# Kernel tuning notes

Measured on AMD Instinct MI355X. Metric: run time of the kernel, lower is better.

## Reference

```python
import jax, jax.numpy as jnp
import numpy as np

D = 128; T = 128; E = 100; H = 2
B = 2048; N0 = 3 * B; K0 = 5; N1 = N0 * K0; K1 = 10
NN = 200000; M = 4096; MSG = 2 * D + E + T  # 484


def t2v(t, w, b):
    # Time2Vec: cos(t * w + b), output [..., T]
    return jnp.cos(t[..., None] * w + b)


def gru_cell(x, h, Wih, bih, Whh, bhh):
    gi = x @ Wih.T + bih
    gh = h @ Whh.T + bhh
    ir, iz, inn = jnp.split(gi, 3, axis=-1)
    hr, hz, hn = jnp.split(gh, 3, axis=-1)
    r = jax.nn.sigmoid(ir + hr)
    u = jax.nn.sigmoid(iz + hz)
    n = jnp.tanh(inn + r * hn)
    return (1.0 - u) * n + u * h


def temporal_attn(node_feat, time_feat, edge_feat, nbr_feat, nbr_time_feat, mask,
                  Wq, bq, Wk, bk, Wv, bv, Wo, bo):
    N = node_feat.shape[0]
    q = (jnp.concatenate([node_feat, time_feat], -1) @ Wq + bq).reshape(N, H, D // H)
    kin = jnp.concatenate([nbr_feat, edge_feat, nbr_time_feat], -1)  # [N, K, D+E+T]
    k = (kin @ Wk + bk).reshape(N, -1, H, D // H)
    v = (kin @ Wv + bv).reshape(N, -1, H, D // H)
    s = jnp.einsum('nhd,nkhd->nhk', q, k) / jnp.sqrt(jnp.asarray(D // H, q.dtype))
    s = jnp.where(mask[:, None, :] > 0, s, jnp.asarray(-1e9, s.dtype))
    a = jax.nn.softmax(s, axis=-1)
    hout = jnp.einsum('nhk,nkhd->nhd', a, v).reshape(N, D)
    return jax.nn.relu(jnp.concatenate([hout, node_feat], -1) @ Wo + bo)


def setup_inputs() -> dict:
    key = jax.random.key(0)
    ks = jax.random.split(key, 60)
    it = iter(range(60))
    nx = lambda: ks[next(it)]
    p = lambda shape: jax.random.normal(nx(), shape, jnp.float32) * 0.05
    inp = dict(memory=p((NN, D)), time_w=p((T,)), time_b=p((T,)),
               gru_Wih=p((3 * D, MSG)), gru_bih=p((3 * D,)),
               gru_Whh=p((3 * D, D)), gru_bhh=p((3 * D,)))
    for l in (0, 1):
        inp['Wq%d' % l] = p((D + T, D)); inp['bq%d' % l] = p((D,))
        inp['Wk%d' % l] = p((D + E + T, D)); inp['bk%d' % l] = p((D,))
        inp['Wv%d' % l] = p((D + E + T, D)); inp['bv%d' % l] = p((D,))
        inp['Wo%d' % l] = p((2 * D, D)); inp['bo%d' % l] = p((D,))
    inp.update(lp_Ws=p((D, D)), lp_bs=p((D,)), lp_Wd=p((D, D)), lp_bd=p((D,)),
               lp_Wo=p((D, 1)), lp_bo=p((1,)))
    inp['msgs'] = jax.random.normal(nx(), (M, MSG), jnp.float32)
    inp['times0'] = jax.random.uniform(nx(), (N0,), jnp.float32) * 100.0 + 100.0
    inp['nbr_times0'] = inp['times0'][:, None] - jax.random.uniform(nx(), (N0, K0), jnp.float32) * 100.0
    inp['nbr_feats0'] = jax.random.normal(nx(), (N0, K0, E), jnp.float32)
    inp['times1'] = jax.random.uniform(nx(), (N1,), jnp.float32) * 100.0 + 100.0
    inp['nbr_times1'] = inp['times1'][:, None] - jax.random.uniform(nx(), (N1, K1), jnp.float32) * 100.0
    inp['nbr_feats1'] = jax.random.normal(nx(), (N1, K1, E), jnp.float32)
    inp['msg_nids'] = jax.random.permutation(nx(), NN)[:M].astype(jnp.int32)
    inp['seed0'] = jax.random.randint(nx(), (N0,), 0, NN, jnp.int32)
    inp['seed1'] = jax.random.randint(nx(), (N1,), 0, NN, jnp.int32)
    inp['nbr_local0'] = (N0 + jax.random.randint(nx(), (N0, K0), 0, N1)).astype(jnp.int32)
    inp['nbr_mask0'] = jax.random.randint(nx(), (N0, K0), 0, 2, jnp.int32).at[:, 0].set(1)
    inp['nbr_mask1'] = jax.random.randint(nx(), (N1, K1), 0, 2, jnp.int32).at[:, 0].set(1)
    inp['src_local'] = jax.random.randint(nx(), (B,), 0, N0, jnp.int32)
    inp['dst_local'] = jax.random.randint(nx(), (B,), 0, N0, jnp.int32)
    inp['neg_local'] = jax.random.randint(nx(), (B,), 0, N0, jnp.int32)
    return inp


def reference(memory, time_w, time_b, gru_Wih, gru_bih, gru_Whh, gru_bhh,
              Wq0, bq0, Wk0, bk0, Wv0, bv0, Wo0, bo0,
              Wq1, bq1, Wk1, bk1, Wv1, bv1, Wo1, bo1,
              lp_Ws, lp_bs, lp_Wd, lp_bd, lp_Wo, lp_bo,
              msgs, times0, nbr_times0, nbr_feats0, times1, nbr_times1, nbr_feats1,
              msg_nids, seed0, seed1, nbr_local0, nbr_mask0, nbr_mask1,
              src_local, dst_local, neg_local):
    # GRU memory update on aggregated messages (get_updated_memory)
    mem = memory.at[msg_nids].set(
        gru_cell(msgs, memory[msg_nids], gru_Wih, gru_bih, gru_Whh, gru_bhh))
    z = jnp.zeros((N0 + N1, D), jnp.float32)
    # hop 1 (outermost): neighbor node features are zeros
    tf1 = t2v(jnp.zeros((N1,), jnp.float32), time_w, time_b)
    ntf1 = t2v(times1[:, None] - nbr_times1, time_w, time_b)
    out1 = temporal_attn(mem[seed1], tf1, nbr_feats1,
                         jnp.zeros((N1, K1, D), jnp.float32), ntf1, nbr_mask1,
                         Wq1, bq1, Wk1, bk1, Wv1, bv1, Wo1, bo1)
    z = z.at[N0 + jnp.arange(N1)].set(out1)
    # hop 0: gather neighbor embeddings from hop-1 results
    tf0 = t2v(jnp.zeros((N0,), jnp.float32), time_w, time_b)
    ntf0 = t2v(times0[:, None] - nbr_times0, time_w, time_b)
    out0 = temporal_attn(mem[seed0], tf0, nbr_feats0, z[nbr_local0], ntf0, nbr_mask0,
                         Wq0, bq0, Wk0, bk0, Wv0, bv0, Wo0, bo0)
    z = z.at[jnp.arange(N0)].set(out0)
    z_src, z_dst, z_neg = z[src_local], z[dst_local], z[neg_local]

    def link_pred(a, c):
        hh = jax.nn.relu(a @ lp_Ws + lp_bs + c @ lp_Wd + lp_bd)
        return jax.nn.sigmoid(hh @ lp_Wo + lp_bo).ravel()

    return link_pred(z_src, z_dst), link_pred(z_src, z_neg)
```

## Files before the change

kernel.cpp:

```cpp
#include <hip/hip_runtime.h>
#include <math.h>

#define D    128
#define TT   128
#define E    100
#define NHD  2
#define BSZ  2048
#define N0C  6144
#define K0C  5
#define N1C  30720
#define K1C  10
#define NNC  200000
#define MC   4096
#define MSG  484
#define KIN  356
#define GK   612
#define GKP  616
#define GN   512

typedef __attribute__((ext_vector_type(8))) short short8v;
typedef __attribute__((ext_vector_type(4))) float f32x4;

__device__ __forceinline__ float sigmoidf_(float x){ return 1.f/(1.f+__expf(-x)); }
__device__ __forceinline__ unsigned short f2b(float f){
    unsigned int x = __float_as_uint(f);
    unsigned int r = (x + 0x7fffu + ((x>>16)&1u)) >> 16;
    return (unsigned short)r;
}
__device__ __forceinline__ float b2f(unsigned short u){
    return __uint_as_float(((unsigned int)u)<<16);
}
__device__ __forceinline__ void pin4(float4& v){
    float a=v.x, b=v.y, c=v.z, d=v.w;
    asm volatile("" : "+v"(a), "+v"(b), "+v"(c), "+v"(d));
    v.x=a; v.y=b; v.z=c; v.w=d;
}

__global__ void k_pre_small(const float* time_b,
                            const float* Wq0,const float* bq0,const float* Wq1,const float* bq1,
                            const float* bv0,const float* Wo0,const float* bo0,
                            const float* bv1,const float* Wo1,const float* bo1,
                            const float* bih,const float* bhh,float* gBias,
                            float* qc0, float* qc1, float* cb0, float* cb1){
    __shared__ float cosb[TT];
    int j = threadIdx.x;
    if(j < TT) cosb[j] = cosf(time_b[j]);
    __syncthreads();
    if(j < 128){
        float a0=bq0[j], a1=bq1[j];
        for(int t=0;t<TT;++t){ a0 += cosb[t]*Wq0[(D+t)*D + j]; a1 += cosb[t]*Wq1[(D+t)*D + j]; }
        qc0[j]=a0; qc1[j]=a1;
        float c0=bo0[j], c1=bo1[j];
        for(int jp=0;jp<D;++jp){ c0 += bv0[jp]*Wo0[jp*D + j]; c1 += bv1[jp]*Wo1[jp*D + j]; }
        cb0[j]=c0; cb1[j]=c1;
    }
    if(j < GN){
        float v;
        if(j < 256)      v = bih[j] + bhh[j];
        else if(j < 384) v = bih[j];
        else             v = bhh[j-128];
        gBias[j] = v;
    }
}

__global__ void k_wf(const float* Wq,const float* Wk,const float* bk,const float* qc,
                     unsigned short* WF, float* cF, int cmin){
    int span = 356 - cmin;
    int hstr = span + 4;
    int width = 2*hstr;
    int idx = blockIdx.x;
    int h = idx / hstr; int cl = idx % hstr;
    int k = threadIdx.x;
    if(cl > span){
        WF[(size_t)k*width + idx] = (unsigned short)0;
        if(k==0) cF[idx] = 0.f;
        return;
    }
    int c = cmin + cl;
    float a = 0.f;
    for(int d=0; d<64; ++d){
        float wkv = (c < KIN) ? Wk[c*D + h*64+d] : bk[h*64+d];
        a += Wq[k*D + h*64+d] * wkv;
    }
    WF[(size_t)k*width + idx] = f2b(a);
    if(k==0){
        float s=0.f;
        for(int d=0; d<64; ++d){
            float wkv = (c < KIN) ? Wk[c*D + h*64+d] : bk[h*64+d];
            s += qc[h*64+d]*wkv;
        }
        cF[idx] = s;
    }
}

__global__ void k_bcat(const float* Wv, const float* Wo, unsigned short* Bcat, int cmin){
    int span = KIN - cmin; int rows = 2*span;
    int r = blockIdx.x; int j = threadIdx.x;
    float a;
    if(r < rows){
        int h = r/span; int c = cmin + (r - h*span);
        a = 0.f;
        for(int d=0; d<64; ++d) a += Wv[c*D + h*64+d] * Wo[(h*64+d)*D + j];
    } else {
        a = Wo[(size_t)(D + (r - rows))*D + j];
    }
    Bcat[(size_t)r*D + j] = f2b(a);
}

__global__ __launch_bounds__(256) void k_gruB(const float* Wih, const float* Whh, unsigned short* B){
    __shared__ float tile[64][65];
    int rb = blockIdx.x*64;
    int jb = blockIdx.y*64;
    int t = threadIdx.x;
    int rr = t&63, jj0 = t>>6;
    #pragma unroll
    for(int i=0;i<16;++i){
        int jj = jj0 + i*4;
        int j = jb + jj; int r = rb + rr;
        float v = 0.f;
        if(r < GK){
            if(j < 256)      v = (r<MSG)? Wih[(size_t)j*MSG+r] : Whh[(size_t)j*D + (r-MSG)];
            else if(j < 384) v = (r<MSG)? Wih[(size_t)j*MSG+r] : 0.f;
            else             v = (r<MSG)? 0.f : Whh[(size_t)(j-128)*D + (r-MSG)];
        }
        tile[jj][rr] = v;
    }
    __syncthreads();
    int jw = t&63, rr0 = t>>6;
    #pragma unroll
    for(int i=0;i<16;++i){
        int rr2 = rr0 + i*4;
        int r = rb + rr2;
        if(r < GK) B[(size_t)r*GN + jb + jw] = f2b(tile[jw][rr2]);
    }
}
__global__ void k_acvt(const float* msgs, const float* memory, const int* msg_nids,
                       unsigned short* ab, float* hprevf, int* map){
    int i = blockIdx.x*256 + threadIdx.x;
    if(i >= MC*GKP) return;
    int row = i / GKP; int c = i - row*GKP;
    if(c == 0) map[msg_nids[row]] = row;
    float v;
    if(c < MSG) v = msgs[(size_t)row*MSG + c];
    else if(c < GK){ int d = c-MSG; v = memory[(size_t)msg_nids[row]*D + d]; hprevf[row*D+d] = v; }
    else v = 0.f;
    ab[i] = f2b(v);
}
__global__ void k_gates3(const float* part, const float* bias, const float* hprevf, float* upd){
    int i = blockIdx.x*256 + threadIdx.x;
    if(i >= MC*D) return;
    int row = i>>7, d = i&127;
    const float* p = part + (size_t)row*GN;
    const size_t S = (size_t)MC*GN;
    float gr = p[d]     + p[S+d]     + p[2*S+d]     + bias[d];
    float gu = p[128+d] + p[S+128+d] + p[2*S+128+d] + bias[128+d];
    float gi = p[256+d] + p[S+256+d] + p[2*S+256+d] + bias[256+d];
    float gh = p[384+d] + p[S+384+d] + p[2*S+384+d] + bias[384+d];
    float r = sigmoidf_(gr);
    float u = sigmoidf_(gu);
    float n = tanhf(gi + r*gh);
    upd[i] = (1.f-u)*n + u*hprevf[i];
}

__global__ void k_gatherf(const int* seed1,const int* seed0,const int* map,const int* msg_nids,
                          const float* memory,const float* upd,
                          unsigned short* hb1, unsigned short* acat1,
                          unsigned short* hb0, unsigned short* acat0){
    int i = blockIdx.x*256 + threadIdx.x;
    const int total1 = N1C*D;
    int li; const int* seed; unsigned short* hb; unsigned short* acat; int ldav, hoff;
    if(i < total1){ li=i; seed=seed1; hb=hb1; acat=acat1; ldav=584; hoff=456; }
    else { li = i - total1; if(li >= N0C*D) return; seed=seed0; hb=hb0; acat=acat0; ldav=840; hoff=712; }
    int row = li>>7, c = li&127;
    int sid = seed[row];
    int mi = map[sid];
    bool valid = ((unsigned)mi < (unsigned)MC) && (msg_nids[mi] == sid);
    float v = valid ? upd[(size_t)mi*D + c] : memory[(size_t)sid*D + c];
    unsigned short u = f2b(v);
    hb[li] = u;
    acat[(size_t)row*ldav + hoff + c] = u;
}

template<int BM, int SPLITK, bool RELU, bool OUTF32>
__global__ __launch_bounds__(256) void k_gmm(const unsigned short* A, int lda,
                                             const unsigned short* B, int ldb,
                                             const float* bias, void* Cp, int ldc,
                                             int K, int N, int M){
    constexpr int ASTR = 72;
    constexpr int BSTR = 72;
    constexpr int RPW = BM/4;
    constexpr int RT  = RPW/16;
    constexpr int AIT = BM/32;
    __shared__ unsigned short As[BM*ASTR];
    __shared__ unsigned short Bs[64*BSTR];
    int t = threadIdx.x;
    int wave = t>>6, lane = t&63;
    int l15 = lane&15, l4 = lane>>4;
    int m0 = blockIdx.y*BM, n0 = blockIdx.x*64;
    int ntiles = (K+63)>>6;
    int tbeg, tend;
    if(SPLITK==1){ tbeg=0; tend=ntiles; }
    else {
        int tper = (ntiles + SPLITK-1)/SPLITK;
        tbeg = blockIdx.z*tper;
        tend = min(ntiles, tbeg+tper);
    }
    f32x4 acc[RT][4];
    #pragma unroll
    for(int rt=0;rt<RT;++rt)
        #pragma unroll
        for(int ct=0;ct<4;++ct) acc[rt][ct] = (f32x4){0.f,0.f,0.f,0.f};

    uint4 apre[AIT]; unsigned short bpre[16];
    auto loadA = [&](int kt){
        int k0 = kt<<6;
        #pragma unroll
        for(int i=0;i<AIT;++i){
            int idx = t + i*256;
            int row = idx>>3; int kc = (idx&7)*8;
            uint4 v = {0u,0u,0u,0u};
            if(k0+kc < K) v = *(const uint4*)(A + (size_t)(m0+row)*lda + k0 + kc);
            apre[i] = v;
        }
    };
    auto loadB = [&](int kt){
        int k0 = kt<<6;
        int n = t&63; int kb = (t>>6)*16;
        int ng = n0+n;
        #pragma unroll
        for(int j=0;j<16;++j){
            int kg = k0 + kb + j;
            bpre[j] = (kg<K && ng<N) ? B[(size_t)kg*ldb + ng] : (unsigned short)0;
        }
    };
    auto stash = [&](){
        #pragma unroll
        for(int i=0;i<AIT;++i){
            int idx = t + i*256;
            int row = idx>>3; int kc = (idx&7)*8;
            *(uint4*)&As[row*ASTR + kc] = apre[i];
        }
        int n = t&63; int kb = (t>>6)*16;
        #pragma unroll
        for(int j=0;j<16;++j) Bs[n*BSTR + kb + j] = bpre[j];
    };

    loadA(tbeg); loadB(tbeg);
    for(int kt=tbeg; kt<tend; ++kt){
        stash();
        __syncthreads();
        if(kt+1 < tend){ loadA(kt+1); loadB(kt+1); }
        #pragma unroll
        for(int kk=0; kk<64; kk+=32){
            short8v bfr[4];
            #pragma unroll
            for(int ct=0;ct<4;++ct)
                bfr[ct] = *(const short8v*)&Bs[(ct*16+l15)*BSTR + kk + l4*8];
            #pragma unroll
            for(int rt=0;rt<RT;++rt){
                short8v afr = *(const short8v*)&As[(wave*RPW + rt*16 + l15)*ASTR + kk + l4*8];
                #pragma unroll
                for(int ct=0;ct<4;++ct)
                    acc[rt][ct] = __builtin_amdgcn_mfma_f32_16x16x32_bf16(afr, bfr[ct], acc[rt][ct], 0,0,0);
            }
        }
        __syncthreads();
    }
    #pragma unroll
    for(int rt=0;rt<RT;++rt){
        #pragma unroll
        for(int ct=0;ct<4;++ct){
            int col = n0 + ct*16 + l15;
            if(col < N){
                #pragma unroll
                for(int r=0;r<4;++r){
                    int row = m0 + wave*RPW + rt*16 + l4*4 + r;
                    if(SPLITK==1){
                        float v = acc[rt][ct][r] + bias[col];
                        if(RELU) v = fmaxf(v, 0.f);
                        if(OUTF32) ((float*)Cp)[(size_t)row*ldc + col] = v;
                        else ((unsigned short*)Cp)[(size_t)row*ldc + col] = f2b(v);
                    } else {
                        ((float*)Cp)[((size_t)blockIdx.z*M + row)*ldc + col] = acc[rt][ct][r];
                    }
                }
            }
        }
    }
}

template<int SPL, bool RELU, bool OUTF32>
__global__ void k_kred(const float* part, int M, int N, const float* bias, void* out){
    int i = blockIdx.x*256 + threadIdx.x;
    if(i >= M*N) return;
    int col = i & (N-1);
    float v = bias[col];
    #pragma unroll
    for(int z=0;z<SPL;++z) v += part[(size_t)z*M*N + i];
    if(RELU) v = fmaxf(v, 0.f);
    if(OUTF32) ((float*)out)[i] = v;
    else ((unsigned short*)out)[i] = f2b(v);
}

template<int K, int CMIN, int S4, int NPW>
__global__ __launch_bounds__(256,4) void k_attn(const unsigned short* __restrict__ qwb,
    unsigned short* __restrict__ avout, int ldav,
    const float* __restrict__ times, const float* __restrict__ nbr_times,
    const float* __restrict__ nbr_feats,
    const int* __restrict__ nbr_mask, const int* __restrict__ nbr_local,
    const unsigned short* __restrict__ zbuf,
    const float* __restrict__ time_w, const float* __restrict__ time_b){
    constexpr int SPAN = KIN - CMIN;
    constexpr int QSTR = SPAN + 4;
    constexpr int QLD  = 2*QSTR;
    int wv = __builtin_amdgcn_readfirstlane(blockIdx.x*4 + (threadIdx.x>>6));
    int lane = threadIdx.x & 63;

    float4 tw4[S4], tb4[S4];
    #pragma unroll
    for(int s=0;s<S4;++s){
        int c = CMIN + s*256 + lane*4;
        if(c >= D+E && c < KIN){
            tw4[s] = *(const float4*)(time_w + (c-(D+E)));
            tb4[s] = *(const float4*)(time_b + (c-(D+E)));
        } else {
            tw4[s] = make_float4(0.f,0.f,0.f,0.f);
            tb4[s] = make_float4(0.f,0.f,0.f,0.f);
        }
    }

    #pragma unroll
    for(int i=0;i<NPW;++i){
        int n = wv*NPW + i;
        const unsigned short* qrow = qwb + (size_t)n*QLD;
        float tn = times[n];
        int   mk[K]; float tk[K]; int nl[K];
        #pragma unroll
        for(int k=0;k<K;++k){
            mk[k] = nbr_mask [(size_t)n*K + k];
            tk[k] = nbr_times[(size_t)n*K + k];
            nl[k] = (CMIN==0) ? nbr_local[(size_t)n*K + k] : 0;
        }

        float4 qw4[NHD][S4]; float qb[NHD];
        #pragma unroll
        for(int h=0;h<NHD;++h){
            qb[h] = b2f(qrow[h*QSTR + SPAN]);
            #pragma unroll
            for(int s=0;s<S4;++s){
                int cl = s*256 + lane*4;
                float4 v = make_float4(0.f,0.f,0.f,0.f);
                if(cl < SPAN){
                    uint2 wq = *(const uint2*)(qrow + h*QSTR + cl);
                    v.x = __uint_as_float(wq.x<<16);
                    v.y = __uint_as_float(wq.x & 0xffff0000u);
                    v.z = __uint_as_float(wq.y<<16);
                    v.w = __uint_as_float(wq.y & 0xffff0000u);
                }
                pin4(v);
                qw4[h][s] = v;
            }
        }

        float4 kin4[K][S4];
        #pragma unroll
        for(int k=0;k<K;++k){
            int gk = (mk[k] > 0) ? k : 0;
            float dt = tn - tk[gk];
            const float* ef = nbr_feats + (size_t)(n*K+gk)*E;
            const unsigned short* zf = (CMIN==0) ?
                (zbuf + (size_t)(nl[gk] - N0C)*D) : (const unsigned short*)0;
            #pragma unroll
            for(int s=0;s<S4;++s){
                int c = CMIN + s*256 + lane*4;
                float4 kv = make_float4(0.f,0.f,0.f,0.f);
                if(c < KIN){
                    if(CMIN==0 && c < D){
                        uint2 wz = *(const uint2*)(zf + c);
                        kv.x = __uint_as_float(wz.x<<16);
                        kv.y = __uint_as_float(wz.x & 0xffff0000u);
                        kv.z = __uint_as_float(wz.y<<16);
                        kv.w = __uint_as_float(wz.y & 0xffff0000u);
                    } else if(c < D+E){
                        kv = *(const float4*)(ef + (c-D));
                    } else {
                        kv.x = __cosf(dt*tw4[s].x + tb4[s].x);
                        kv.y = __cosf(dt*tw4[s].y + tb4[s].y);
                        kv.z = __cosf(dt*tw4[s].z + tb4[s].z);
                        kv.w = __cosf(dt*tw4[s].w + tb4[s].w);
                    }
                }
                pin4(kv);
                kin4[k][s] = kv;
            }
        }

        float p0[K], p1[K];
        #pragma unroll
        for(int k=0;k<K;++k){ p0[k]=0.f; p1[k]=0.f; }
        #pragma unroll
        for(int k=0;k<K;++k){
            if(mk[k] > 0){
                float a0 = 0.f, a1 = 0.f;
                #pragma unroll
                for(int s=0;s<S4;++s){
                    float4 kv = kin4[k][s];
                    a0 += kv.x*qw4[0][s].x + kv.y*qw4[0][s].y + kv.z*qw4[0][s].z + kv.w*qw4[0][s].w;
                    a1 += kv.x*qw4[1][s].x + kv.y*qw4[1][s].y + kv.z*qw4[1][s].z + kv.w*qw4[1][s].w;
                }
                p0[k] = a0; p1[k] = a1;
            }
        }

        #pragma unroll
        for(int off=32; off; off>>=1){
            #pragma unroll
            for(int k=0;k<K;++k){
                if(mk[k] > 0){
                    p0[k] += __shfl_xor(p0[k], off);
                    p1[k] += __shfl_xor(p1[k], off);
                }
            }
        }

        float sval[NHD][K];
        #pragma unroll
        for(int k=0;k<K;++k){
            bool act = mk[k] > 0;
            sval[0][k] = act ? (p0[k] + qb[0])*0.125f : -1e9f;
            sval[1][k] = act ? (p1[k] + qb[1])*0.125f : -1e9f;
        }
        #pragma unroll
        for(int h=0;h<NHD;++h){
            float mx = -1e30f;
            #pragma unroll
            for(int k=0;k<K;++k) mx = fmaxf(mx, sval[h][k]);
            float z=0.f;
            #pragma unroll
            for(int k=0;k<K;++k){ float e = __expf(sval[h][k]-mx); sval[h][k]=e; z+=e; }
            float inv = 1.f/z;
            #pragma unroll
            for(int k=0;k<K;++k) sval[h][k]*=inv;
        }

        #pragma unroll
        for(int s=0;s<S4;++s){
            int cl = s*256 + lane*4;
            if(cl < SPAN){
                float a00=0.f,a01=0.f,a02=0.f,a03=0.f;
                float a10=0.f,a11=0.f,a12=0.f,a13=0.f;
                #pragma unroll
                for(int k=0;k<K;++k){
                    if(mk[k] > 0){
                        float4 kv = kin4[k][s];
                        float w0 = sval[0][k], w1 = sval[1][k];
                        a00 += w0*kv.x; a01 += w0*kv.y; a02 += w0*kv.z; a03 += w0*kv.w;
                        a10 += w1*kv.x; a11 += w1*kv.y; a12 += w1*kv.z; a13 += w1*kv.w;
                    }
                }
                uint2 o0, o1;
                o0.x = (unsigned int)f2b(a00) | ((unsigned int)f2b(a01)<<16);
                o0.y = (unsigned int)f2b(a02) | ((unsigned int)f2b(a03)<<16);
                o1.x = (unsigned int)f2b(a10) | ((unsigned int)f2b(a11)<<16);
                o1.y = (unsigned int)f2b(a12) | ((unsigned int)f2b(a13)<<16);
                *(uint2*)(avout + (size_t)n*ldav + cl)        = o0;
                *(uint2*)(avout + (size_t)n*ldav + SPAN + cl) = o1;
            }
        }
    }
}

__global__ __launch_bounds__(128) void k_linkpred(const float* z0,
      const int* src,const int* dst,const int* neg,
      const float* Ws,const float* bs,const float* Wd,const float* bd,
      const float* Wo,const float* bo, float* out){
    __shared__ float zs[D], zd[D], zn[D];
    __shared__ float red[4];
    int b = blockIdx.x; int d = threadIdx.x;
    zs[d] = z0[(size_t)src[b]*D + d];
    zd[d] = z0[(size_t)dst[b]*D + d];
    zn[d] = z0[(size_t)neg[b]*D + d];
    __syncthreads();
    float ss=0.f, sdd=0.f, snn=0.f;
    for(int c=0;c<D;++c){
        float w1 = Ws[c*D + d], w2 = Wd[c*D + d];
        ss  += zs[c]*w1; sdd += zd[c]*w2; snn += zn[c]*w2;
    }
    float bb = bs[d] + bd[d];
    float h1 = fmaxf(ss + sdd + bb, 0.f);
    float h2 = fmaxf(ss + snn + bb, 0.f);
    float w = Wo[d];
    float v1 = h1*w, v2 = h2*w;
    #pragma unroll
    for(int off=32; off; off>>=1){ v1 += __shfl_xor(v1,off); v2 += __shfl_xor(v2,off); }
    int wid = d>>6;
    if((d&63)==0){ red[wid*2]=v1; red[wid*2+1]=v2; }
    __syncthreads();
    if(d==0){
        out[b]       = sigmoidf_(red[0]+red[2] + bo[0]);
        out[BSZ + b] = sigmoidf_(red[1]+red[3] + bo[0]);
    }
}

extern "C" void kernel_launch(void* const* d_in, const int* in_sizes, int n_in,
                              void* d_out, int out_size, void* d_ws, size_t ws_size,
                              hipStream_t stream) {
    const float* memory  = (const float*)d_in[0];
    const float* time_w  = (const float*)d_in[1];
    const float* time_b  = (const float*)d_in[2];
    const float* gWih    = (const float*)d_in[3];
    const float* gbih    = (const float*)d_in[4];
    const float* gWhh    = (const float*)d_in[5];
    const float* gbhh    = (const float*)d_in[6];
    const float* Wq0=(const float*)d_in[7],  *bq0=(const float*)d_in[8];
    const float* Wk0=(const float*)d_in[9],  *bk0=(const float*)d_in[10];
    const float* Wv0=(const float*)d_in[11], *bv0=(const float*)d_in[12];
    const float* Wo0=(const float*)d_in[13], *bo0=(const float*)d_in[14];
    const float* Wq1=(const float*)d_in[15], *bq1=(const float*)d_in[16];
    const float* Wk1=(const float*)d_in[17], *bk1=(const float*)d_in[18];
    const float* Wv1=(const float*)d_in[19], *bv1=(const float*)d_in[20];
    const float* Wo1=(const float*)d_in[21], *bo1=(const float*)d_in[22];
    const float* lpWs=(const float*)d_in[23], *lpbs=(const float*)d_in[24];
    const float* lpWd=(const float*)d_in[25], *lpbd=(const float*)d_in[26];
    const float* lpWo=(const float*)d_in[27], *lpbo=(const float*)d_in[28];
    const float* msgs    = (const float*)d_in[29];
    const float* times0  = (const float*)d_in[30];
    const float* ntimes0 = (const float*)d_in[31];
    const float* nfeats0 = (const float*)d_in[32];
    const float* times1  = (const float*)d_in[33];
    const float* ntimes1 = (const float*)d_in[34];
    const float* nfeats1 = (const float*)d_in[35];
    const int* msg_nids  = (const int*)d_in[36];
    const int* seed0     = (const int*)d_in[37];
    const int* seed1     = (const int*)d_in[38];
    const int* nbr_local0= (const int*)d_in[39];
    const int* nbr_mask0 = (const int*)d_in[40];
    const int* nbr_mask1 = (const int*)d_in[41];
    const int* src       = (const int*)d_in[42];
    const int* dst       = (const int*)d_in[43];
    const int* neg       = (const int*)d_in[44];

    char* ws = (char*)d_ws;
    size_t off = 0;
    auto alloc = [&](size_t bytes)->char*{
        char* p = ws + off;
        off += (bytes + 255) & ~(size_t)255;
        return p;
    };
    int*   map   = (int*)  alloc((size_t)NNC*4);
    float* upd   = (float*)alloc((size_t)MC*D*4);
    unsigned short* hb1   = (unsigned short*)alloc((size_t)N1C*D*2);
    unsigned short* qwb1  = (unsigned short*)alloc((size_t)N1C*464*2);
    unsigned short* acat1 = (unsigned short*)alloc((size_t)N1C*584*2);
    unsigned short* zb1   = (unsigned short*)alloc((size_t)N1C*D*2);
    unsigned short* hb0   = (unsigned short*)alloc((size_t)N0C*D*2);
    unsigned short* qwb0  = (unsigned short*)alloc((size_t)N0C*720*2);
    unsigned short* acat0 = (unsigned short*)alloc((size_t)N0C*840*2);
    float* z0    = (float*)alloc((size_t)N0C*D*4);
    float* qc0   = (float*)alloc(512);
    float* qc1   = (float*)alloc(512);
    float* cb0   = (float*)alloc(512);
    float* cb1   = (float*)alloc(512);
    unsigned short* WFb0 = (unsigned short*)alloc((size_t)D*720*2);
    unsigned short* WFb1 = (unsigned short*)alloc((size_t)D*464*2);
    float* cF0   = (float*)alloc((size_t)720*4);
    float* cF1   = (float*)alloc((size_t)464*4);
    unsigned short* Bcat1 = (unsigned short*)alloc((size_t)584*D*2);
    unsigned short* Bcat0 = (unsigned short*)alloc((size_t)840*D*2);
    unsigned short* gA    = (unsigned short*)alloc((size_t)MC*GKP*2);
    unsigned short* gB    = (unsigned short*)alloc((size_t)GK*GN*2);
    float* gBias = (float*)alloc((size_t)GN*4);
    float* hprevf= (float*)alloc((size_t)MC*D*4);
    float* part  = (float*)alloc((size_t)2*N1C*D*4);
    float* outp = (float*)d_out;

    k_pre_small<<<1,512,0,stream>>>(time_b, Wq0,bq0,Wq1,bq1, bv0,Wo0,bo0, bv1,Wo1,bo1,
                                    gbih, gbhh, gBias, qc0,qc1,cb0,cb1);
    k_wf<<<720,128,0,stream>>>(Wq0,Wk0,bk0,qc0, WFb0,cF0, 0);
    k_wf<<<464,128,0,stream>>>(Wq1,Wk1,bk1,qc1, WFb1,cF1, 128);
    k_bcat<<<584,128,0,stream>>>(Wv1, Wo1, Bcat1, 128);
    k_bcat<<<840,128,0,stream>>>(Wv0, Wo0, Bcat0, 0);
    k_gruB<<<dim3(10,8),256,0,stream>>>(gWih, gWhh, gB);

    k_acvt<<<(MC*GKP+255)/256,256,0,stream>>>(msgs, memory, msg_nids, gA, hprevf, map);
    k_gmm<128,3,false,true><<<dim3(GN/64, MC/128, 3),256,0,stream>>>(gA,GKP, gB,GN, gBias, part,GN, GK, GN, MC);
    k_gates3<<<(MC*D+255)/256,256,0,stream>>>(part, gBias, hprevf, upd);

    k_gatherf<<<((N1C+N0C)*D)/256,256,0,stream>>>(seed1, seed0, map, msg_nids, memory, upd,
                                                  hb1, acat1, hb0, acat0);

    k_gmm<128,1,false,false><<<dim3(8,  N1C/128),256,0,stream>>>(hb1,128, WFb1,464, cF1, qwb1,464, 128, 464, N1C);
    k_gmm<128,1,false,false><<<dim3(12, N0C/128),256,0,stream>>>(hb0,128, WFb0,720, cF0, qwb0,720, 128, 720, N0C);

    k_attn<K1C,128,1,1><<<N1C/4,256,0,stream>>>(qwb1, acat1, 584, times1, ntimes1, nfeats1,
                                                nbr_mask1, (const int*)0, (const unsigned short*)0,
                                                time_w, time_b);
    k_gmm<128,2,true,false><<<dim3(2, N1C/128, 2),256,0,stream>>>(acat1,584, Bcat1,D, cb1, part,D, 584, D, N1C);
    k_kred<2,true,false><<<(N1C*D+255)/256,256,0,stream>>>(part, N1C, D, cb1, zb1);

    k_attn<K0C,0,2,1><<<N0C/4,256,0,stream>>>(qwb0, acat0, 840, times0, ntimes0, nfeats0,
                                              nbr_mask0, nbr_local0, zb1,
                                              time_w, time_b);
    k_gmm<64,4,true,true><<<dim3(2, N0C/64, 4),256,0,stream>>>(acat0,840, Bcat0,D, cb0, part,D, 840, D, N0C);
    k_kred<4,true,true><<<(N0C*D+255)/256,256,0,stream>>>(part, N0C, D, cb0, z0);

    k_linkpred<<<BSZ,128,0,stream>>>(z0, src,dst,neg, lpWs,lpbs,lpWd,lpbd, lpWo,lpbo, outp);
}
```

Before: 583.4 us.

## Simplify attention kernel register use and drop split-K for hop-1 output GEMM

```diff
diff --git a/kernel.cpp b/kernel.cpp
--- a/kernel.cpp
+++ b/kernel.cpp
@@ -29,11 +29,6 @@
 }
 __device__ __forceinline__ float b2f(unsigned short u){
     return __uint_as_float(((unsigned int)u)<<16);
-}
-__device__ __forceinline__ void pin4(float4& v){
-    float a=v.x, b=v.y, c=v.z, d=v.w;
-    asm volatile("" : "+v"(a), "+v"(b), "+v"(c), "+v"(d));
-    v.x=a; v.y=b; v.z=c; v.w=d;
 }
 
 __global__ void k_pre_small(const float* time_b,
@@ -303,7 +298,7 @@
 }
 
 template<int K, int CMIN, int S4, int NPW>
-__global__ __launch_bounds__(256,4) void k_attn(const unsigned short* __restrict__ qwb,
+__global__ __launch_bounds__(256) void k_attn(const unsigned short* __restrict__ qwb,
     unsigned short* __restrict__ avout, int ldav,
     const float* __restrict__ times, const float* __restrict__ nbr_times,
     const float* __restrict__ nbr_feats,
@@ -357,7 +352,6 @@
                     v.z = __uint_as_float(wq.y<<16);
                     v.w = __uint_as_float(wq.y & 0xffff0000u);
                 }
-                pin4(v);
                 qw4[h][s] = v;
             }
         }
@@ -365,11 +359,10 @@
         float4 kin4[K][S4];
         #pragma unroll
         for(int k=0;k<K;++k){
-            int gk = (mk[k] > 0) ? k : 0;
-            float dt = tn - tk[gk];
-            const float* ef = nbr_feats + (size_t)(n*K+gk)*E;
+            float dt = tn - tk[k];
+            const float* ef = nbr_feats + (size_t)(n*K+k)*E;
             const unsigned short* zf = (CMIN==0) ?
-                (zbuf + (size_t)(nl[gk] - N0C)*D) : (const unsigned short*)0;
+                (zbuf + (size_t)(nl[k] - N0C)*D) : (const unsigned short*)0;
             #pragma unroll
             for(int s=0;s<S4;++s){
                 int c = CMIN + s*256 + lane*4;
@@ -390,36 +383,29 @@
                         kv.w = __cosf(dt*tw4[s].w + tb4[s].w);
                     }
                 }
-                pin4(kv);
                 kin4[k][s] = kv;
             }
         }
 
         float p0[K], p1[K];
         #pragma unroll
-        for(int k=0;k<K;++k){ p0[k]=0.f; p1[k]=0.f; }
-        #pragma unroll
         for(int k=0;k<K;++k){
-            if(mk[k] > 0){
-                float a0 = 0.f, a1 = 0.f;
-                #pragma unroll
-                for(int s=0;s<S4;++s){
-                    float4 kv = kin4[k][s];
-                    a0 += kv.x*qw4[0][s].x + kv.y*qw4[0][s].y + kv.z*qw4[0][s].z + kv.w*qw4[0][s].w;
-                    a1 += kv.x*qw4[1][s].x + kv.y*qw4[1][s].y + kv.z*qw4[1][s].z + kv.w*qw4[1][s].w;
-                }
-                p0[k] = a0; p1[k] = a1;
-            }
+            float a0 = 0.f, a1 = 0.f;
+            #pragma unroll
+            for(int s=0;s<S4;++s){
+                float4 kv = kin4[k][s];
+                a0 += kv.x*qw4[0][s].x + kv.y*qw4[0][s].y + kv.z*qw4[0][s].z + kv.w*qw4[0][s].w;
+                a1 += kv.x*qw4[1][s].x + kv.y*qw4[1][s].y + kv.z*qw4[1][s].z + kv.w*qw4[1][s].w;
+            }
+            p0[k] = a0; p1[k] = a1;
         }
 
         #pragma unroll
         for(int off=32; off; off>>=1){
             #pragma unroll
             for(int k=0;k<K;++k){
-                if(mk[k] > 0){
-                    p0[k] += __shfl_xor(p0[k], off);
-                    p1[k] += __shfl_xor(p1[k], off);
-                }
+                p0[k] += __shfl_xor(p0[k], off);
+                p1[k] += __shfl_xor(p1[k], off);
             }
         }
 
@@ -442,31 +428,25 @@
             #pragma unroll
             for(int k=0;k<K;++k) sval[h][k]*=inv;
         }
-
-        #pragma unroll
-        for(int s=0;s<S4;++s){
+        #pragma unroll
+        for(int h=0;h<NHD;++h)
+          #pragma unroll
+          for(int s=0;s<S4;++s){
             int cl = s*256 + lane*4;
             if(cl < SPAN){
-                float a00=0.f,a01=0.f,a02=0.f,a03=0.f;
-                float a10=0.f,a11=0.f,a12=0.f,a13=0.f;
+                float v0=0.f,v1=0.f,v2=0.f,v3=0.f;
                 #pragma unroll
                 for(int k=0;k<K;++k){
-                    if(mk[k] > 0){
-                        float4 kv = kin4[k][s];
-                        float w0 = sval[0][k], w1 = sval[1][k];
-                        a00 += w0*kv.x; a01 += w0*kv.y; a02 += w0*kv.z; a03 += w0*kv.w;
-                        a10 += w1*kv.x; a11 += w1*kv.y; a12 += w1*kv.z; a13 += w1*kv.w;
-                    }
+                    float a = sval[h][k];
+                    v0 += a*kin4[k][s].x; v1 += a*kin4[k][s].y;
+                    v2 += a*kin4[k][s].z; v3 += a*kin4[k][s].w;
                 }
-                uint2 o0, o1;
-                o0.x = (unsigned int)f2b(a00) | ((unsigned int)f2b(a01)<<16);
-                o0.y = (unsigned int)f2b(a02) | ((unsigned int)f2b(a03)<<16);
-                o1.x = (unsigned int)f2b(a10) | ((unsigned int)f2b(a11)<<16);
-                o1.y = (unsigned int)f2b(a12) | ((unsigned int)f2b(a13)<<16);
-                *(uint2*)(avout + (size_t)n*ldav + cl)        = o0;
-                *(uint2*)(avout + (size_t)n*ldav + SPAN + cl) = o1;
-            }
-        }
+                uint2 o;
+                o.x = (unsigned int)f2b(v0) | ((unsigned int)f2b(v1)<<16);
+                o.y = (unsigned int)f2b(v2) | ((unsigned int)f2b(v3)<<16);
+                *(uint2*)(avout + (size_t)n*ldav + h*SPAN + cl) = o;
+            }
+          }
     }
 }
 
@@ -595,8 +575,7 @@
     k_attn<K1C,128,1,1><<<N1C/4,256,0,stream>>>(qwb1, acat1, 584, times1, ntimes1, nfeats1,
                                                 nbr_mask1, (const int*)0, (const unsigned short*)0,
                                                 time_w, time_b);
-    k_gmm<128,2,true,false><<<dim3(2, N1C/128, 2),256,0,stream>>>(acat1,584, Bcat1,D, cb1, part,D, 584, D, N1C);
-    k_kred<2,true,false><<<(N1C*D+255)/256,256,0,stream>>>(part, N1C, D, cb1, zb1);
+    k_gmm<128,1,true,false><<<dim3(2, N1C/128),256,0,stream>>>(acat1,584, Bcat1,D, cb1, zb1,D, 584, D, N1C);
 
     k_attn<K0C,0,2,1><<<N0C/4,256,0,stream>>>(qwb0, acat0, 840, times0, ntimes0, nfeats0,
                                               nbr_mask0, nbr_local0, zb1,
```

Result: faster. 543.9 us (-6.8%).
